# Kernel tuning notes

Measured on AMD Instinct MI355X. Metric: run time of the kernel, lower is better.

Reference implementation:

```python
import jax, jax.numpy as jnp
import numpy as np

N = 1_000_000   # total cluster nodes
D = 128         # input_dim
B = 4096        # number of scenes (segments)
M = 1024        # rows in dist embeddings


def setup_inputs() -> dict:
    key = jax.random.key(0)
    ks = jax.random.split(key, 16)
    inp = {
        "x_clu": jax.random.normal(ks[0], (N, D), dtype=jnp.float32),
        "mask_clu": jax.random.bernoulli(ks[1], 0.9, (N,)),
        "batch_clu": jnp.sort(jax.random.randint(ks[2], (N,), 0, B, dtype=jnp.int32)),
        "dist_embedding": jax.random.normal(ks[3], (M, 6), dtype=jnp.float32),
        "dist_embedding_norm": jax.random.normal(ks[4], (M, 1), dtype=jnp.float32),
        # AttentionalAggregation gate: Linear(D, 1)
        "gate_w": jax.random.normal(ks[5], (D, 1), dtype=jnp.float32) / np.sqrt(D),
        "gate_b": jnp.zeros((1,), dtype=jnp.float32),
        # vel_si_vec MLP [D, D, 6]
        "w1": jax.random.normal(ks[6], (D, D), dtype=jnp.float32) / np.sqrt(D),
        "b1": jnp.zeros((D,), dtype=jnp.float32),
        "w2": jax.random.normal(ks[7], (D, 6), dtype=jnp.float32) / np.sqrt(D),
        "b2": jnp.zeros((6,), dtype=jnp.float32),
        # vel_si_norm MLP [D, D, 1]
        "w1n": jax.random.normal(ks[8], (D, D), dtype=jnp.float32) / np.sqrt(D),
        "b1n": jnp.zeros((D,), dtype=jnp.float32),
        "w2n": jax.random.normal(ks[9], (D, 1), dtype=jnp.float32) / np.sqrt(D),
        "b2n": jnp.zeros((1,), dtype=jnp.float32),
    }
    return inp


def _attn_pool(x, mask, seg, gate_w, gate_b):
    # gate logits for every node; masked nodes excluded from the segment softmax
    gate = jnp.einsum("nd,do->n", x, gate_w) + gate_b[0]           # [N]
    neg = jnp.finfo(gate.dtype).min
    gate = jnp.where(mask, gate, neg)
    gmax = jax.ops.segment_max(gate, seg, num_segments=B)          # [B]
    e = jnp.where(mask, jnp.exp(gate - gmax[seg]), 0.0)            # [N]
    denom = jax.ops.segment_sum(e, seg, num_segments=B)            # [B]
    w = e / jnp.maximum(denom[seg], 1e-12)                         # [N]
    return jax.ops.segment_sum(w[:, None] * x, seg, num_segments=B)  # [B, D]


def reference(x_clu, mask_clu, batch_clu, dist_embedding, dist_embedding_norm,
              gate_w, gate_b, w1, b1, w2, b2, w1n, b1n, w2n, b2n):
    x_scene = _attn_pool(x_clu, mask_clu, batch_clu, gate_w, gate_b)  # [B, D]
    vel = jax.nn.relu(x_scene @ w1 + b1) @ w2 + b2                    # [B, 6]
    nrm = jax.nn.relu(x_scene @ w1n + b1n) @ w2n + b2n                # [B, 1]
    out_vec = vel * jnp.mean(dist_embedding, axis=0)                  # [B, 6]
    out_norm = nrm * jnp.mean(dist_embedding_norm, axis=0)            # [B, 1]
    return out_vec, out_norm
```

## Files before the change

### kernel.cpp

```cpp
#include <hip/hip_runtime.h>

#define D 128

__global__ void means_kernel(const float* __restrict__ de, const float* __restrict__ den,
                             int M, float* __restrict__ out7) {
    __shared__ float sm[256][8];
    float a[7];
#pragma unroll
    for (int j = 0; j < 7; ++j) a[j] = 0.f;
    for (int r = threadIdx.x; r < M; r += 256) {
#pragma unroll
        for (int j = 0; j < 6; ++j) a[j] += de[r * 6 + j];
        a[6] += den[r];
    }
#pragma unroll
    for (int j = 0; j < 7; ++j) sm[threadIdx.x][j] = a[j];
    __syncthreads();
    for (int s = 128; s > 0; s >>= 1) {
        if (threadIdx.x < (unsigned)s) {
#pragma unroll
            for (int j = 0; j < 7; ++j) sm[threadIdx.x][j] += sm[threadIdx.x + s][j];
        }
        __syncthreads();
    }
    if (threadIdx.x < 7) out7[threadIdx.x] = sm[0][threadIdx.x] / (float)M;
}

__global__ void bounds_kernel(const int* __restrict__ seg, int N, int B,
                              int* __restrict__ off) {
    int i = blockIdx.x * blockDim.x + threadIdx.x;
    if (i > N) return;
    int cur  = (i < N) ? seg[i]     : B;
    int prev = (i > 0) ? seg[i - 1] : -1;
    for (int j = prev + 1; j <= cur; ++j) off[j] = i;
}

__global__ void pool_mlp_kernel(const float* __restrict__ x, const int* __restrict__ mask,
                                const int* __restrict__ off,
                                const float* __restrict__ gate_w, const float* __restrict__ gate_b,
                                const float* __restrict__ w1, const float* __restrict__ b1,
                                const float* __restrict__ w2, const float* __restrict__ b2,
                                const float* __restrict__ w1n, const float* __restrict__ b1n,
                                const float* __restrict__ w2n, const float* __restrict__ b2n,
                                const float* __restrict__ means,
                                float* __restrict__ out_vec, float* __restrict__ out_norm) {
    const int b    = blockIdx.x;
    const int tid  = threadIdx.x;
    const int wv   = tid >> 6;
    const int lane = tid & 63;
    const int q    = lane >> 4;
    const int l16  = lane & 15;
    const int part = (wv << 2) | q;

    const int start = off[b];
    const int end   = off[b + 1];

    const float4 gwA = ((const float4*)gate_w)[l16];
    const float4 gwB = ((const float4*)gate_w)[16 + l16];
    const float  gb  = gate_b[0];

    float  s    = 0.f;
    float4 accA = {0.f, 0.f, 0.f, 0.f};
    float4 accB = {0.f, 0.f, 0.f, 0.f};

    const int last = end - 1;
#pragma unroll 2
    for (int i = start; i < end; i += 16) {
        const int row = i + (wv << 2) + q;
        const int r   = min(row, last);
        const float* xr = x + (size_t)r * D;
        const float4 xa = ((const float4*)xr)[l16];
        const float4 xb = ((const float4*)xr)[16 + l16];
        const int    mk = mask[r];
        float p = xa.x * gwA.x + xa.y * gwA.y + xa.z * gwA.z + xa.w * gwA.w
                + xb.x * gwB.x + xb.y * gwB.y + xb.z * gwB.z + xb.w * gwB.w;
#pragma unroll
        for (int o = 8; o > 0; o >>= 1) p += __shfl_xor(p, o);
        const float e = (row < end && mk != 0) ? __expf(p + gb) : 0.f;
        s     += e;
        accA.x += e * xa.x; accA.y += e * xa.y; accA.z += e * xa.z; accA.w += e * xa.w;
        accB.x += e * xb.x; accB.y += e * xb.y; accB.z += e * xb.z; accB.w += e * xb.w;
    }

    __shared__ float sacc[16][D + 4];
    __shared__ float ss[16];
    *(float4*)&sacc[part][l16 * 4]      = accA;
    *(float4*)&sacc[part][64 + l16 * 4] = accB;
    if (l16 == 0) ss[part] = s;
    __syncthreads();

    __shared__ float xs[D];
    if (tid < D) {
        float S = 0.f, A = 0.f;
#pragma unroll
        for (int h = 0; h < 16; ++h) { S += ss[h]; A += sacc[h][tid]; }
        xs[tid] = A / fmaxf(S, 1e-12f);
    }
    __syncthreads();

    __shared__ float hid[D], hidn[D];
    if (tid < D) {
        float a1 = b1[tid];
#pragma unroll 8
        for (int i = 0; i < D; ++i) a1 += xs[i] * w1[i * D + tid];
        hid[tid] = fmaxf(a1, 0.f);
    } else {
        const int h = tid - D;
        float a1n = b1n[h];
#pragma unroll 8
        for (int i = 0; i < D; ++i) a1n += xs[i] * w1n[i * D + h];
        hidn[h] = fmaxf(a1n, 0.f);
    }
    __syncthreads();

    if (tid < 112) {
        const int g = tid >> 4, l = tid & 15;
        float o = 0.f;
        if (g < 6) {
#pragma unroll
            for (int k = 0; k < 8; ++k) { const int i = l * 8 + k; o += hid[i] * w2[i * 6 + g]; }
        } else {
#pragma unroll
            for (int k = 0; k < 8; ++k) { const int i = l * 8 + k; o += hidn[i] * w2n[i]; }
        }
#pragma unroll
        for (int of = 8; of > 0; of >>= 1) o += __shfl_xor(o, of);
        if (l == 0) {
            if (g < 6) out_vec[b * 6 + g] = (o + b2[g]) * means[g];
            else       out_norm[b]        = (o + b2n[0]) * means[6];
        }
    }
}

extern "C" void kernel_launch(void* const* d_in, const int* in_sizes, int n_in,
                              void* d_out, int out_size, void* d_ws, size_t ws_size,
                              hipStream_t stream) {
    const float* x      = (const float*)d_in[0];
    const int*   mask   = (const int*)  d_in[1];
    const int*   seg    = (const int*)  d_in[2];
    const float* de     = (const float*)d_in[3];
    const float* den    = (const float*)d_in[4];
    const float* gate_w = (const float*)d_in[5];
    const float* gate_b = (const float*)d_in[6];
    const float* w1     = (const float*)d_in[7];
    const float* b1     = (const float*)d_in[8];
    const float* w2     = (const float*)d_in[9];
    const float* b2     = (const float*)d_in[10];
    const float* w1n    = (const float*)d_in[11];
    const float* b1n    = (const float*)d_in[12];
    const float* w2n    = (const float*)d_in[13];
    const float* b2n    = (const float*)d_in[14];

    const int N  = in_sizes[1];
    const int M  = in_sizes[4];
    const int Bn = out_size / 7;

    float* means    = (float*)d_ws;
    int*   off      = (int*)d_ws + 16;
    float* out_vec  = (float*)d_out;
    float* out_norm = (float*)d_out + (size_t)Bn * 6;

    means_kernel<<<1, 256, 0, stream>>>(de, den, M, means);
    bounds_kernel<<<(N + 256) / 256, 256, 0, stream>>>(seg, N, Bn, off);
    pool_mlp_kernel<<<Bn, 256, 0, stream>>>(x, mask, off, gate_w, gate_b,
                                            w1, b1, w2, b2, w1n, b1n, w2n, b2n,
                                            means, out_vec, out_norm);
}
```

Before: 693.9 us.

## Split segment pooling across two blocks and move MLP to separate combine kernel

The fused pool+MLP kernel is split in two. A streaming kernel launches two blocks per segment that interleave 16-row chunks and write unnormalized partial sums to workspace. A second kernel combines the two partials and runs the MLP. This doubles the number of blocks streaming x and keeps the MLP tail off the bandwidth-bound phase, at the cost of an extra launch and a partials round trip through global memory.

```diff
diff --git a/kernel.cpp b/kernel.cpp
--- a/kernel.cpp
+++ b/kernel.cpp
@@ -35,16 +35,12 @@
     for (int j = prev + 1; j <= cur; ++j) off[j] = i;
 }
 
-__global__ void pool_mlp_kernel(const float* __restrict__ x, const int* __restrict__ mask,
-                                const int* __restrict__ off,
-                                const float* __restrict__ gate_w, const float* __restrict__ gate_b,
-                                const float* __restrict__ w1, const float* __restrict__ b1,
-                                const float* __restrict__ w2, const float* __restrict__ b2,
-                                const float* __restrict__ w1n, const float* __restrict__ b1n,
-                                const float* __restrict__ w2n, const float* __restrict__ b2n,
-                                const float* __restrict__ means,
-                                float* __restrict__ out_vec, float* __restrict__ out_norm) {
-    const int b    = blockIdx.x;
+__global__ void stream_kernel(const float* __restrict__ x, const int* __restrict__ mask,
+                              const int* __restrict__ off,
+                              const float* __restrict__ gate_w, const float* __restrict__ gate_b,
+                              float* __restrict__ partials) {
+    const int b    = blockIdx.x >> 1;
+    const int h    = blockIdx.x & 1;
     const int tid  = threadIdx.x;
     const int wv   = tid >> 6;
     const int lane = tid & 63;
@@ -62,10 +58,10 @@
     float  s    = 0.f;
     float4 accA = {0.f, 0.f, 0.f, 0.f};
     float4 accB = {0.f, 0.f, 0.f, 0.f};
+    const int last = end - 1;
 
-    const int last = end - 1;
-#pragma unroll 2
-    for (int i = start; i < end; i += 16) {
+#pragma unroll 4
+    for (int i = start + (h << 4); i < end; i += 32) {
         const int row = i + (wv << 2) + q;
         const int r   = min(row, last);
         const float* xr = x + (size_t)r * D;
@@ -77,7 +73,7 @@
 #pragma unroll
         for (int o = 8; o > 0; o >>= 1) p += __shfl_xor(p, o);
         const float e = (row < end && mk != 0) ? __expf(p + gb) : 0.f;
-        s     += e;
+        s      += e;
         accA.x += e * xa.x; accA.y += e * xa.y; accA.z += e * xa.z; accA.w += e * xa.w;
         accB.x += e * xb.x; accB.y += e * xb.y; accB.z += e * xb.z; accB.w += e * xb.w;
     }
@@ -89,12 +85,36 @@
     if (l16 == 0) ss[part] = s;
     __syncthreads();
 
+    float* outp = partials + (size_t)blockIdx.x * 132;
+    if (tid < D) {
+        float A = 0.f;
+#pragma unroll
+        for (int k = 0; k < 16; ++k) A += sacc[k][tid];
+        outp[tid] = A;
+    } else if (tid == D) {
+        float S = 0.f;
+#pragma unroll
+        for (int k = 0; k < 16; ++k) S += ss[k];
+        outp[D] = S;
+    }
+}
+
+__global__ void combine_mlp_kernel(const float* __restrict__ partials,
+                                   const float* __restrict__ w1, const float* __restrict__ b1,
+                                   const float* __restrict__ w2, const float* __restrict__ b2,
+                                   const float* __restrict__ w1n, const float* __restrict__ b1n,
+                                   const float* __restrict__ w2n, const float* __restrict__ b2n,
+                                   const float* __restrict__ means,
+                                   float* __restrict__ out_vec, float* __restrict__ out_norm) {
+    const int b   = blockIdx.x;
+    const int tid = threadIdx.x;
+    const float* p0 = partials + (size_t)(2 * b) * 132;
+    const float* p1 = p0 + 132;
+
     __shared__ float xs[D];
     if (tid < D) {
-        float S = 0.f, A = 0.f;
-#pragma unroll
-        for (int h = 0; h < 16; ++h) { S += ss[h]; A += sacc[h][tid]; }
-        xs[tid] = A / fmaxf(S, 1e-12f);
+        const float S = fmaxf(p0[D] + p1[D], 1e-12f);
+        xs[tid] = (p0[tid] + p1[tid]) / S;
     }
     __syncthreads();
 
@@ -105,11 +125,11 @@
         for (int i = 0; i < D; ++i) a1 += xs[i] * w1[i * D + tid];
         hid[tid] = fmaxf(a1, 0.f);
     } else {
-        const int h = tid - D;
-        float a1n = b1n[h];
+        const int hh = tid - D;
+        float a1n = b1n[hh];
 #pragma unroll 8
-        for (int i = 0; i < D; ++i) a1n += xs[i] * w1n[i * D + h];
-        hidn[h] = fmaxf(a1n, 0.f);
+        for (int i = 0; i < D; ++i) a1n += xs[i] * w1n[i * D + hh];
+        hidn[hh] = fmaxf(a1n, 0.f);
     }
     __syncthreads();
 
@@ -157,12 +177,14 @@
 
     float* means    = (float*)d_ws;
     int*   off      = (int*)d_ws + 16;
+    float* partials = (float*)d_ws + 8192;
     float* out_vec  = (float*)d_out;
     float* out_norm = (float*)d_out + (size_t)Bn * 6;
 
     means_kernel<<<1, 256, 0, stream>>>(de, den, M, means);
     bounds_kernel<<<(N + 256) / 256, 256, 0, stream>>>(seg, N, Bn, off);
-    pool_mlp_kernel<<<Bn, 256, 0, stream>>>(x, mask, off, gate_w, gate_b,
-                                            w1, b1, w2, b2, w1n, b1n, w2n, b2n,
-                                            means, out_vec, out_norm);
+    stream_kernel<<<2 * Bn, 256, 0, stream>>>(x, mask, off, gate_w, gate_b, partials);
+    combine_mlp_kernel<<<Bn, 256, 0, stream>>>(partials, w1, b1, w2, b2,
+                                               w1n, b1n, w2n, b2n, means,
+                                               out_vec, out_norm);
 }
```

Result: slower. 708.6 us (+2.1%).
